# Performance work log

Measured on AMD Instinct MI355X. Metric: run time of the kernel, lower is better.

The kernel has to match this reference:

```python
import jax, jax.numpy as jnp
import numpy as np

UNITS = 128
D_FEAT = 128
B, N = 4, 4096
EDGE_PROB = 0.01  # avg in-degree ~ N * EDGE_PROB ~ 41


def setup_inputs() -> dict:
    key = jax.random.key(0)
    k1, k2, k3, k4 = jax.random.split(key, 4)
    x = jax.random.normal(k1, (B, N, D_FEAT), dtype=jnp.float32)
    # binary adjacency mask, as consumed by tf.where(adj)
    adj = (jax.random.uniform(k2, (B, N, N)) < EDGE_PROB).astype(jnp.float32)
    # Dense(units, use_bias=False) kernels: msg on concat(x_snd, x_rec) -> [2d, U];
    # node_update on concat(x, messages) -> [d+U, U]
    W_msg = (jax.random.normal(k3, (2 * D_FEAT, UNITS), dtype=jnp.float32)
             / np.sqrt(2 * D_FEAT).astype(np.float32))
    W_upd = (jax.random.normal(k4, (D_FEAT + UNITS, UNITS), dtype=jnp.float32)
             / np.sqrt(D_FEAT + UNITS).astype(np.float32))
    return {"x": x, "adj": adj, "W_msg": W_msg, "W_upd": W_upd}


def reference(x, adj, W_msg, W_upd):
    # Faithful to MPNN2.call: edges are (b, s, r) where adj[b, s, r] != 0.
    # message per edge = concat(x[b,s], x[b,r]) @ W_msg = x[b,s]@Ws + x[b,r]@Wr.
    # messages[b,r] = segment_mean over incoming edges. Since the receiver term
    # x[b,r]@Wr is identical for all edges into r, its mean is itself, and the
    # sender term's mean is (adj^T @ (x@Ws)) / in_degree. Empty segments -> 0
    # (tf.math.unsorted_segment_mean semantics). This avoids data-dependent
    # edge-list shapes and is jit-compatible.
    d = x.shape[-1]
    Ws, Wr = W_msg[:d], W_msg[d:]          # [d, U] each
    xs = x @ Ws                            # sender contribution  [B, N, U]
    xr = x @ Wr                            # receiver contribution [B, N, U]
    deg = jnp.einsum('bsr->br', adj)[..., None]          # in-degree [B, N, 1]
    snd_sum = jnp.einsum('bsr,bsu->bru', adj, xs)        # [B, N, U]
    messages = jnp.where(deg > 0,
                         snd_sum / jnp.maximum(deg, 1.0) + xr,
                         0.0)
    # node_update on concat(x, messages); activation=None, use_bias=False
    return jnp.concatenate([x, messages], axis=-1) @ W_upd
```

## Files before the change

### kernel.cpp

```cpp
#include <hip/hip_runtime.h>

#define BB 4
#define NN 4096

typedef __attribute__((ext_vector_type(8))) short short8;
typedef __attribute__((ext_vector_type(4))) float f32x4;

__device__ __forceinline__ unsigned short f2bf(float f) {
    union { float f; unsigned int i; } cv; cv.f = f;
    unsigned int i = cv.i;
    return (unsigned short)((i + 0x7FFFu + ((i >> 16) & 1u)) >> 16);
}
__device__ __forceinline__ float asf(unsigned int u) {
    union { unsigned int i; float f; } cv; cv.i = u; return cv.f;
}

__global__ __launch_bounds__(256) void kA(const float* __restrict__ adj,
                                          const float* __restrict__ Wmsg,
                                          const float* __restrict__ Wupd,
                                          unsigned short* __restrict__ WcatT,
                                          unsigned long long* __restrict__ bitT) {
    __shared__ float fS[128], fR[128];
    int bid = blockIdx.x, t = threadIdx.x;
    if (bid < 128) {
        int k = bid;
        if (t < 128) { fS[t] = Wmsg[k * 128 + t]; fR[t] = Wmsg[(128 + k) * 128 + t]; }
        __syncthreads();
        if (t < 128) {
            float a1 = 0.f, a2 = 0.f;
#pragma unroll 8
            for (int m = 0; m < 128; ++m) {
                float wu = Wupd[(128 + m) * 128 + t];
                a1 += fS[m] * wu;
                a2 += fR[m] * wu;
            }
            WcatT[(size_t)t * 128 + k]         = f2bf(Wupd[k * 128 + t]);
            WcatT[(size_t)(128 + t) * 128 + k] = f2bf(a2);
            WcatT[(size_t)(256 + t) * 128 + k] = f2bf(a1);
        }
    }
    int b  = bid >> 8;
    int s0 = (bid & 255) * 16;
    int wv = t >> 6, l = t & 63;
    const float* ab = adj + ((size_t)b * NN + s0) * NN + wv * 1024 + l * 4;
    unsigned long long* bt = bitT + ((size_t)(b * NN + s0) << 6);
    for (int i = 0; i < 16; i += 4) {
        float4 v0[4], v1[4], v2[4], v3[4];
#pragma unroll
        for (int it = 0; it < 4; ++it) {
            v0[it] = *(const float4*)(ab + (size_t)(i + 0) * NN + it * 256);
            v1[it] = *(const float4*)(ab + (size_t)(i + 1) * NN + it * 256);
            v2[it] = *(const float4*)(ab + (size_t)(i + 2) * NN + it * 256);
            v3[it] = *(const float4*)(ab + (size_t)(i + 3) * NN + it * 256);
        }
#pragma unroll
        for (int u = 0; u < 4; ++u) {
            float4* v = (u == 0) ? v0 : (u == 1) ? v1 : (u == 2) ? v2 : v3;
            int row = i + u;
#pragma unroll
            for (int it = 0; it < 4; ++it) {
                unsigned long long m0 = __ballot(v[it].x != 0.0f);
                unsigned long long m1 = __ballot(v[it].y != 0.0f);
                unsigned long long m2 = __ballot(v[it].z != 0.0f);
                unsigned long long m3 = __ballot(v[it].w != 0.0f);
                if (l < 4) {
                    unsigned long long wd = (l == 0) ? m0 : (l == 1) ? m1 : (l == 2) ? m2 : m3;
                    bt[((size_t)row << 6) + (wv * 4 + it) * 4 + l] = wd;
                }
            }
        }
    }
}

__global__ __launch_bounds__(256) void kB(const float* __restrict__ X,
                                          const unsigned short* __restrict__ WcatT,
                                          float* __restrict__ TD,
                                          unsigned short* __restrict__ YB) {
    int bid = blockIdx.x, t = threadIdx.x;
    int m0 = (bid & 255) * 64;
    int nb = bid >> 8;
    int lane = t & 63, wave = t >> 6;
    int quad = lane >> 4, lr = lane & 15;
    const float* xr = X + (size_t)(m0 + wave * 16 + lr) * 128;

    auto LOADA = [&](int KK) -> short8 {
        float4 f0 = *(const float4*)(xr + KK * 32 + quad * 8);
        float4 f1 = *(const float4*)(xr + KK * 32 + quad * 8 + 4);
        short8 av;
        av[0] = (short)f2bf(f0.x); av[1] = (short)f2bf(f0.y);
        av[2] = (short)f2bf(f0.z); av[3] = (short)f2bf(f0.w);
        av[4] = (short)f2bf(f1.x); av[5] = (short)f2bf(f1.y);
        av[6] = (short)f2bf(f1.z); av[7] = (short)f2bf(f1.w);
        return av;
    };
    short8 a0 = LOADA(0), a1 = LOADA(1), a2 = LOADA(2), a3 = LOADA(3);

    f32x4 acc[8];
#pragma unroll
    for (int s = 0; s < 8; ++s) acc[s] = (f32x4)0.f;

    const unsigned short* wbase = WcatT + ((size_t)nb << 14) + (size_t)lr * 128 + quad * 8;
#pragma unroll
    for (int kk = 0; kk < 4; ++kk) {
        short8 a = (kk == 0) ? a0 : (kk == 1) ? a1 : (kk == 2) ? a2 : a3;
#pragma unroll
        for (int s = 0; s < 8; ++s) {
            short8 bf = *(const short8*)(wbase + (size_t)(s * 16) * 128 + kk * 32);
            acc[s] = __builtin_amdgcn_mfma_f32_16x16x32_bf16(a, bf, acc[s], 0, 0, 0);
        }
    }
    if (nb == 2) {
#pragma unroll
        for (int s = 0; s < 8; ++s)
#pragma unroll
            for (int r = 0; r < 4; ++r) {
                int row = m0 + wave * 16 + quad * 4 + r;
                YB[(size_t)row * 128 + s * 16 + lr] = f2bf(acc[s][r]);
            }
    } else {
#pragma unroll
        for (int s = 0; s < 8; ++s)
#pragma unroll
            for (int r = 0; r < 4; ++r) {
                int row = m0 + wave * 16 + quad * 4 + r;
                TD[(size_t)row * 256 + nb * 128 + s * 16 + lr] = acc[s][r];
            }
    }
}

__global__ __launch_bounds__(256) void kC(const unsigned long long* __restrict__ bitT,
                                          const unsigned int* __restrict__ YB32,
                                          const float* __restrict__ TD,
                                          float* __restrict__ out) {
    __shared__ int cnt[16];
    __shared__ unsigned short list[16][128];
    int bid  = blockIdx.x, t = threadIdx.x;
    int b    = bid >> 8;
    int rg16 = bid & 255;
    if (t < 16) cnt[t] = 0;
    __syncthreads();

    int g  = rg16 >> 4;
    int l0 = (rg16 & 15) * 4;
    const unsigned long long* bt = bitT + ((size_t)(b * NN) << 6) + (g << 2);
    for (int i = 0; i < NN / 256; ++i) {
        int s = t + 256 * i;
        const unsigned long long* p = bt + ((size_t)s << 6);
        unsigned long long w0 = p[0], w1 = p[1], w2 = p[2], w3 = p[3];
        unsigned n0 = (unsigned)(w0 >> l0) & 0xFu;
        unsigned n1 = (unsigned)(w1 >> l0) & 0xFu;
        unsigned n2 = (unsigned)(w2 >> l0) & 0xFu;
        unsigned n3 = (unsigned)(w3 >> l0) & 0xFu;
        while (n0) { int i2 = __ffs(n0) - 1; n0 &= n0 - 1; int c = 4 * i2;     int sl = atomicAdd(&cnt[c], 1); if (sl < 128) list[c][sl] = (unsigned short)s; }
        while (n1) { int i2 = __ffs(n1) - 1; n1 &= n1 - 1; int c = 4 * i2 + 1; int sl = atomicAdd(&cnt[c], 1); if (sl < 128) list[c][sl] = (unsigned short)s; }
        while (n2) { int i2 = __ffs(n2) - 1; n2 &= n2 - 1; int c = 4 * i2 + 2; int sl = atomicAdd(&cnt[c], 1); if (sl < 128) list[c][sl] = (unsigned short)s; }
        while (n3) { int i2 = __ffs(n3) - 1; n3 &= n3 - 1; int c = 4 * i2 + 3; int sl = atomicAdd(&cnt[c], 1); if (sl < 128) list[c][sl] = (unsigned short)s; }
    }
    __syncthreads();

    int lane = t & 63, w = t >> 6;
    const unsigned int* yb = YB32 + ((size_t)b << 18) + lane;
    for (int q = 0; q < 4; ++q) {
        int c   = w * 4 + q;
        int rgl = b * NN + rg16 * 16 + c;
        int deg = cnt[c];
        int ctot = min(deg, 128);
        const float2* td = (const float2*)(TD + (size_t)rgl * 256);
        float2 t1 = td[lane];
        float2 res = t1;
        if (deg > 0) {
            float al0 = 0.f, ah0 = 0.f, al1 = 0.f, ah1 = 0.f;
            float al2 = 0.f, ah2 = 0.f, al3 = 0.f, ah3 = 0.f;
            const unsigned short* ls = list[c];
            int e = 0;
            for (; e + 4 <= ctot; e += 4) {
                int s0 = ls[e], s1 = ls[e + 1], s2 = ls[e + 2], s3 = ls[e + 3];
                unsigned u0 = yb[(size_t)s0 << 6];
                unsigned u1 = yb[(size_t)s1 << 6];
                unsigned u2 = yb[(size_t)s2 << 6];
                unsigned u3 = yb[(size_t)s3 << 6];
                al0 += asf(u0 << 16); ah0 += asf(u0 & 0xffff0000u);
                al1 += asf(u1 << 16); ah1 += asf(u1 & 0xffff0000u);
                al2 += asf(u2 << 16); ah2 += asf(u2 & 0xffff0000u);
                al3 += asf(u3 << 16); ah3 += asf(u3 & 0xffff0000u);
            }
            for (; e < ctot; ++e) {
                unsigned u = yb[(size_t)ls[e] << 6];
                al0 += asf(u << 16); ah0 += asf(u & 0xffff0000u);
            }
            float inv = 1.0f / (float)deg;
            float2 d2 = td[64 + lane];
            res.x = t1.x + d2.x + (al0 + al1 + al2 + al3) * inv;
            res.y = t1.y + d2.y + (ah0 + ah1 + ah2 + ah3) * inv;
        }
        ((float2*)(out + (size_t)rgl * 128))[lane] = res;
    }
}

extern "C" void kernel_launch(void* const* d_in, const int* in_sizes, int n_in,
                              void* d_out, int out_size, void* d_ws, size_t ws_size,
                              hipStream_t stream) {
    const float* x    = (const float*)d_in[0];
    const float* adj  = (const float*)d_in[1];
    const float* Wmsg = (const float*)d_in[2];
    const float* Wupd = (const float*)d_in[3];
    float* out = (float*)d_out;

    char* ws = (char*)d_ws;
    unsigned short*     WcatT = (unsigned short*)(ws);
    float*              TD    = (float*)(ws + 131072);
    unsigned short*     YB    = (unsigned short*)(ws + 131072 + 16777216);
    unsigned long long* bitT  = (unsigned long long*)(ws + 131072 + 16777216 + 4194304);

    kA<<<1024, 256, 0, stream>>>(adj, Wmsg, Wupd, WcatT, bitT);
    kB<<<768, 256, 0, stream>>>(x, WcatT, TD, YB);
    kC<<<1024, 256, 0, stream>>>(bitT, (const unsigned int*)YB, TD, out);
}
```

Before: 430.3 us.

## Fuse dense node-update GEMM into gather kernel and regroup bit-mask layout

The dense TD projection (x times the first two weight blocks) no longer goes through a 16MB global round-trip. Each kC block now computes its 16 rows of TD with MFMA into shared memory, and kB only computes the bf16 sender projection YB. The transposed adjacency bitmask is also laid out group-major, so each kC block reads a contiguous stream of 4-word chunks instead of a strided one. In exchange kC uses 16KB more LDS, which may lower occupancy, and re-reads the weight tile in every block.

```diff
diff --git a/kernel.cpp b/kernel.cpp
--- a/kernel.cpp
+++ b/kernel.cpp
@@ -2,6 +2,7 @@
 
 #define BB 4
 #define NN 4096
+
 
 typedef __attribute__((ext_vector_type(8))) short short8;
 typedef __attribute__((ext_vector_type(4))) float f32x4;
@@ -43,7 +44,7 @@
     int s0 = (bid & 255) * 16;
     int wv = t >> 6, l = t & 63;
     const float* ab = adj + ((size_t)b * NN + s0) * NN + wv * 1024 + l * 4;
-    unsigned long long* bt = bitT + ((size_t)(b * NN + s0) << 6);
+    unsigned long long* btb = bitT + ((size_t)(b * 16)) * NN * 4;
     for (int i = 0; i < 16; i += 4) {
         float4 v0[4], v1[4], v2[4], v3[4];
 #pragma unroll
@@ -56,7 +57,7 @@
 #pragma unroll
         for (int u = 0; u < 4; ++u) {
             float4* v = (u == 0) ? v0 : (u == 1) ? v1 : (u == 2) ? v2 : v3;
-            int row = i + u;
+            int s = s0 + i + u;
 #pragma unroll
             for (int it = 0; it < 4; ++it) {
                 unsigned long long m0 = __ballot(v[it].x != 0.0f);
@@ -65,7 +66,8 @@
                 unsigned long long m3 = __ballot(v[it].w != 0.0f);
                 if (l < 4) {
                     unsigned long long wd = (l == 0) ? m0 : (l == 1) ? m1 : (l == 2) ? m2 : m3;
-                    bt[((size_t)row << 6) + (wv * 4 + it) * 4 + l] = wd;
+                    int g = wv * 4 + it;
+                    btb[((size_t)g * NN + s) * 4 + l] = wd;
                 }
             }
         }
@@ -74,14 +76,13 @@
 
 __global__ __launch_bounds__(256) void kB(const float* __restrict__ X,
                                           const unsigned short* __restrict__ WcatT,
-                                          float* __restrict__ TD,
                                           unsigned short* __restrict__ YB) {
     int bid = blockIdx.x, t = threadIdx.x;
-    int m0 = (bid & 255) * 64;
-    int nb = bid >> 8;
+    int m0 = bid * 64;
     int lane = t & 63, wave = t >> 6;
     int quad = lane >> 4, lr = lane & 15;
     const float* xr = X + (size_t)(m0 + wave * 16 + lr) * 128;
+    const unsigned short* wbase = WcatT + ((size_t)2 << 14) + (size_t)lr * 128 + quad * 8;
 
     auto LOADA = [&](int KK) -> short8 {
         float4 f0 = *(const float4*)(xr + KK * 32 + quad * 8);
@@ -98,8 +99,6 @@
     f32x4 acc[8];
 #pragma unroll
     for (int s = 0; s < 8; ++s) acc[s] = (f32x4)0.f;
-
-    const unsigned short* wbase = WcatT + ((size_t)nb << 14) + (size_t)lr * 128 + quad * 8;
 #pragma unroll
     for (int kk = 0; kk < 4; ++kk) {
         short8 a = (kk == 0) ? a0 : (kk == 1) ? a1 : (kk == 2) ? a2 : a3;
@@ -109,64 +108,92 @@
             acc[s] = __builtin_amdgcn_mfma_f32_16x16x32_bf16(a, bf, acc[s], 0, 0, 0);
         }
     }
-    if (nb == 2) {
-#pragma unroll
-        for (int s = 0; s < 8; ++s)
-#pragma unroll
-            for (int r = 0; r < 4; ++r) {
-                int row = m0 + wave * 16 + quad * 4 + r;
-                YB[(size_t)row * 128 + s * 16 + lr] = f2bf(acc[s][r]);
-            }
-    } else {
-#pragma unroll
-        for (int s = 0; s < 8; ++s)
-#pragma unroll
-            for (int r = 0; r < 4; ++r) {
-                int row = m0 + wave * 16 + quad * 4 + r;
-                TD[(size_t)row * 256 + nb * 128 + s * 16 + lr] = acc[s][r];
-            }
-    }
-}
-
-__global__ __launch_bounds__(256) void kC(const unsigned long long* __restrict__ bitT,
+#pragma unroll
+    for (int s = 0; s < 8; ++s)
+#pragma unroll
+        for (int r = 0; r < 4; ++r) {
+            int row = m0 + wave * 16 + quad * 4 + r;
+            YB[(size_t)row * 128 + s * 16 + lr] = f2bf(acc[s][r]);
+        }
+}
+
+__global__ __launch_bounds__(256) void kC(const float* __restrict__ X,
+                                          const unsigned short* __restrict__ WcatT,
+                                          const unsigned long long* __restrict__ bitT,
                                           const unsigned int* __restrict__ YB32,
-                                          const float* __restrict__ TD,
                                           float* __restrict__ out) {
     __shared__ int cnt[16];
     __shared__ unsigned short list[16][128];
+    __shared__ float TDl[16][256];
     int bid  = blockIdx.x, t = threadIdx.x;
     int b    = bid >> 8;
     int rg16 = bid & 255;
+    int g  = rg16 >> 4;
+    int l0 = (rg16 & 15) * 4;
     if (t < 16) cnt[t] = 0;
     __syncthreads();
 
-    int g  = rg16 >> 4;
-    int l0 = (rg16 & 15) * 4;
-    const unsigned long long* bt = bitT + ((size_t)(b * NN) << 6) + (g << 2);
-    for (int i = 0; i < NN / 256; ++i) {
-        int s = t + 256 * i;
-        const unsigned long long* p = bt + ((size_t)s << 6);
-        unsigned long long w0 = p[0], w1 = p[1], w2 = p[2], w3 = p[3];
-        unsigned n0 = (unsigned)(w0 >> l0) & 0xFu;
-        unsigned n1 = (unsigned)(w1 >> l0) & 0xFu;
-        unsigned n2 = (unsigned)(w2 >> l0) & 0xFu;
-        unsigned n3 = (unsigned)(w3 >> l0) & 0xFu;
-        while (n0) { int i2 = __ffs(n0) - 1; n0 &= n0 - 1; int c = 4 * i2;     int sl = atomicAdd(&cnt[c], 1); if (sl < 128) list[c][sl] = (unsigned short)s; }
-        while (n1) { int i2 = __ffs(n1) - 1; n1 &= n1 - 1; int c = 4 * i2 + 1; int sl = atomicAdd(&cnt[c], 1); if (sl < 128) list[c][sl] = (unsigned short)s; }
-        while (n2) { int i2 = __ffs(n2) - 1; n2 &= n2 - 1; int c = 4 * i2 + 2; int sl = atomicAdd(&cnt[c], 1); if (sl < 128) list[c][sl] = (unsigned short)s; }
-        while (n3) { int i2 = __ffs(n3) - 1; n3 &= n3 - 1; int c = 4 * i2 + 3; int sl = atomicAdd(&cnt[c], 1); if (sl < 128) list[c][sl] = (unsigned short)s; }
+    {
+        const unsigned long long* bt = bitT + ((size_t)(b * 16 + g)) * NN * 4;
+        for (int i = 0; i < NN / 256; ++i) {
+            int s = t + 256 * i;
+            const unsigned long long* p = bt + ((size_t)s << 2);
+            unsigned long long w0 = p[0], w1 = p[1], w2 = p[2], w3 = p[3];
+            unsigned n0 = (unsigned)(w0 >> l0) & 0xFu;
+            unsigned n1 = (unsigned)(w1 >> l0) & 0xFu;
+            unsigned n2 = (unsigned)(w2 >> l0) & 0xFu;
+            unsigned n3 = (unsigned)(w3 >> l0) & 0xFu;
+            while (n0) { int i2 = __ffs(n0) - 1; n0 &= n0 - 1; int c = 4 * i2;     int sl = atomicAdd(&cnt[c], 1); if (sl < 128) list[c][sl] = (unsigned short)s; }
+            while (n1) { int i2 = __ffs(n1) - 1; n1 &= n1 - 1; int c = 4 * i2 + 1; int sl = atomicAdd(&cnt[c], 1); if (sl < 128) list[c][sl] = (unsigned short)s; }
+            while (n2) { int i2 = __ffs(n2) - 1; n2 &= n2 - 1; int c = 4 * i2 + 2; int sl = atomicAdd(&cnt[c], 1); if (sl < 128) list[c][sl] = (unsigned short)s; }
+            while (n3) { int i2 = __ffs(n3) - 1; n3 &= n3 - 1; int c = 4 * i2 + 3; int sl = atomicAdd(&cnt[c], 1); if (sl < 128) list[c][sl] = (unsigned short)s; }
+        }
+    }
+
+    int lane = t & 63, w = t >> 6;
+    int quad = lane >> 4, lr = lane & 15;
+    {
+        int rrow0 = b * NN + rg16 * 16;
+        const float* xr = X + (size_t)(rrow0 + lr) * 128;
+        auto LOADA = [&](int KK) -> short8 {
+            float4 f0 = *(const float4*)(xr + KK * 32 + quad * 8);
+            float4 f1 = *(const float4*)(xr + KK * 32 + quad * 8 + 4);
+            short8 av;
+            av[0] = (short)f2bf(f0.x); av[1] = (short)f2bf(f0.y);
+            av[2] = (short)f2bf(f0.z); av[3] = (short)f2bf(f0.w);
+            av[4] = (short)f2bf(f1.x); av[5] = (short)f2bf(f1.y);
+            av[6] = (short)f2bf(f1.z); av[7] = (short)f2bf(f1.w);
+            return av;
+        };
+        short8 a0 = LOADA(0), a1 = LOADA(1), a2 = LOADA(2), a3 = LOADA(3);
+        f32x4 acc[4];
+#pragma unroll
+        for (int s = 0; s < 4; ++s) acc[s] = (f32x4)0.f;
+        const unsigned short* wbase = WcatT + (size_t)(w * 64 + lr) * 128 + quad * 8;
+#pragma unroll
+        for (int kk = 0; kk < 4; ++kk) {
+            short8 a = (kk == 0) ? a0 : (kk == 1) ? a1 : (kk == 2) ? a2 : a3;
+#pragma unroll
+            for (int s = 0; s < 4; ++s) {
+                short8 bf = *(const short8*)(wbase + (size_t)(s * 16) * 128 + kk * 32);
+                acc[s] = __builtin_amdgcn_mfma_f32_16x16x32_bf16(a, bf, acc[s], 0, 0, 0);
+            }
+        }
+#pragma unroll
+        for (int s = 0; s < 4; ++s)
+#pragma unroll
+            for (int r = 0; r < 4; ++r)
+                TDl[quad * 4 + r][w * 64 + s * 16 + lr] = acc[s][r];
     }
     __syncthreads();
 
-    int lane = t & 63, w = t >> 6;
     const unsigned int* yb = YB32 + ((size_t)b << 18) + lane;
     for (int q = 0; q < 4; ++q) {
         int c   = w * 4 + q;
         int rgl = b * NN + rg16 * 16 + c;
         int deg = cnt[c];
         int ctot = min(deg, 128);
-        const float2* td = (const float2*)(TD + (size_t)rgl * 256);
-        float2 t1 = td[lane];
+        float2 t1 = *(const float2*)&TDl[c][2 * lane];
         float2 res = t1;
         if (deg > 0) {
             float al0 = 0.f, ah0 = 0.f, al1 = 0.f, ah1 = 0.f;
@@ -189,7 +216,7 @@
                 al0 += asf(u << 16); ah0 += asf(u & 0xffff0000u);
             }
             float inv = 1.0f / (float)deg;
-            float2 d2 = td[64 + lane];
+            float2 d2 = *(const float2*)&TDl[c][128 + 2 * lane];
             res.x = t1.x + d2.x + (al0 + al1 + al2 + al3) * inv;
             res.y = t1.y + d2.y + (ah0 + ah1 + ah2 + ah3) * inv;
         }
@@ -208,11 +235,10 @@
 
     char* ws = (char*)d_ws;
     unsigned short*     WcatT = (unsigned short*)(ws);
-    float*              TD    = (float*)(ws + 131072);
-    unsigned short*     YB    = (unsigned short*)(ws + 131072 + 16777216);
-    unsigned long long* bitT  = (unsigned long long*)(ws + 131072 + 16777216 + 4194304);
+    unsigned short*     YB    = (unsigned short*)(ws + 131072);
+    unsigned long long* bitT  = (unsigned long long*)(ws + 131072 + 4194304);
 
     kA<<<1024, 256, 0, stream>>>(adj, Wmsg, Wupd, WcatT, bitT);
-    kB<<<768, 256, 0, stream>>>(x, WcatT, TD, YB);
-    kC<<<1024, 256, 0, stream>>>(bitT, (const unsigned int*)YB, TD, out);
-}
+    kB<<<256, 256, 0, stream>>>(x, WcatT, YB);
+    kC<<<1024, 256, 0, stream>>>(x, WcatT, bitT, (const unsigned int*)YB, out);
+}
```

Measured after the change: 413.3 us. -3.9%, faster.
